# Kernel optimization log

Measured on AMD Instinct MI355X. Metric: run time of the kernel, lower is better.

## Reference

```python
import jax, jax.numpy as jnp
import numpy as np


def _flip_sequences(inputs, lengths):
    # Keeps padding at the end while reversing the valid prefix (per example).
    T = inputs.shape[1]
    def one(x, L):
        return jnp.flip(jnp.roll(x, T - L, axis=0), axis=0)
    return jax.vmap(one)(inputs, lengths)


def _gru_direction(xy, mask, Wi, Wh, bi, bhn):
    # xy: [B,T,D], mask: [B,T] (True = padding -> carry old state)
    B = xy.shape[0]
    H = bhn.shape[0]
    h0 = jnp.zeros((B, H), xy.dtype)
    xs = jnp.moveaxis(xy, 1, 0)    # [T,B,D]
    ms = jnp.moveaxis(mask, 1, 0)  # [T,B]

    def step(h, inp):
        x_t, m_t = inp
        gi = x_t @ Wi + bi          # [B,3H] input projections (r,z,n)
        gh = h @ Wh                 # [B,3H] hidden projections
        gi_r, gi_z, gi_n = jnp.split(gi, 3, axis=-1)
        gh_r, gh_z, gh_n = jnp.split(gh, 3, axis=-1)
        r = jax.nn.sigmoid(gi_r + gh_r)
        z = jax.nn.sigmoid(gi_z + gh_z)
        n = jnp.tanh(gi_n + r * (gh_n + bhn))
        new_h = (1.0 - z) * n + z * h
        h_next = jnp.where(m_t[:, None], h, new_h)  # mask: keep old state on padding
        return h_next, new_h

    _, outs = jax.lax.scan(step, h0, (xs, ms))
    return jnp.moveaxis(outs, 0, 1)  # [B,T,H]


def setup_inputs() -> dict:
    key = jax.random.key(0)
    ks = jax.random.split(key, 12)
    B, T, N, E, H = 256, 1000, 128, 4, 256
    D = N + E
    s = 0.08
    return {
        "spike_inputs": jax.random.normal(ks[0], (B, T, N), jnp.float32),
        "external_inputs": jax.random.normal(ks[1], (B, T, E), jnp.float32),
        "trial_lengths": jax.random.randint(ks[2], (B,), 1, T + 1),
        "Wi_f": jax.random.normal(ks[3], (D, 3 * H), jnp.float32) * s,
        "Wh_f": jax.random.normal(ks[4], (H, 3 * H), jnp.float32) * s,
        "bi_f": jnp.zeros((3 * H,), jnp.float32),
        "bhn_f": jnp.zeros((H,), jnp.float32),
        "Wi_b": jax.random.normal(ks[5], (D, 3 * H), jnp.float32) * s,
        "Wh_b": jax.random.normal(ks[6], (H, 3 * H), jnp.float32) * s,
        "bi_b": jnp.zeros((3 * H,), jnp.float32),
        "bhn_b": jnp.zeros((H,), jnp.float32),
    }


def reference(spike_inputs, external_inputs, trial_lengths,
              Wi_f, Wh_f, bi_f, bhn_f, Wi_b, Wh_b, bi_b, bhn_b):
    B, T = spike_inputs.shape[:2]
    # mask_sequences: True where t >= trial length (padding)
    mask = jnp.arange(T)[None, :] >= trial_lengths[:, None]  # [B,T]

    # forward direction
    xy_f = jnp.concatenate([spike_inputs, external_inputs], axis=-1)
    fwd = _gru_direction(xy_f, mask, Wi_f, Wh_f, bi_f, bhn_f)

    # backward direction on flipped sequences (padding stays at the end,
    # so the padding mask is identical)
    rs = _flip_sequences(spike_inputs, trial_lengths)
    re = _flip_sequences(external_inputs, trial_lengths)
    xy_b = jnp.concatenate([rs, re], axis=-1)
    bwd = _gru_direction(xy_b, mask, Wi_b, Wh_b, bi_b, bhn_b)
    bwd = _flip_sequences(bwd, trial_lengths)

    return jnp.concatenate([fwd, bwd], axis=-1)  # [B,T,2H]
```

## Files before the change

### kernel.cpp

```cpp
#include <hip/hip_runtime.h>

#define T_SEQ 1000
#define NS 128
#define NE 4
#define DIN 132
#define G3 768
#define WGS 512

typedef __attribute__((ext_vector_type(8))) short short8;
typedef __attribute__((ext_vector_type(4))) float floatx4;

#define CNT_OFF 0
#define HX_OFF  131072
#define HX_BYTES (32*2*8192)
#define WS_ZERO_BYTES (HX_OFF + HX_BYTES)

#define MFMA16(a,b,c) __builtin_amdgcn_mfma_f32_16x16x32_bf16((a),(b),(c),0,0,0)

__device__ __forceinline__ unsigned short f2bf(float f){
  unsigned u = __float_as_uint(f);
  return (unsigned short)((u + 0x7FFFu + ((u>>16)&1u)) >> 16);
}
__device__ __forceinline__ float bf2f(unsigned short b){
  return __uint_as_float(((unsigned)b)<<16);
}
__device__ __forceinline__ unsigned long long ld64a(const void* p){
  return __hip_atomic_load((const unsigned long long*)p, __ATOMIC_RELAXED, __HIP_MEMORY_SCOPE_AGENT);
}
__device__ __forceinline__ void st32a(void* p, unsigned v){
  __hip_atomic_store((unsigned*)p, v, __ATOMIC_RELAXED, __HIP_MEMORY_SCOPE_AGENT);
}

__global__ __launch_bounds__(WGS, 1) void bigru3(
  const float* __restrict__ spike, const float* __restrict__ extin,
  const int* __restrict__ lens,
  const float* __restrict__ WiF, const float* __restrict__ WhF,
  const float* __restrict__ biF, const float* __restrict__ bhF,
  const float* __restrict__ WiB, const float* __restrict__ WhB,
  const float* __restrict__ biB, const float* __restrict__ bhB,
  float* __restrict__ out,
  unsigned* __restrict__ cnt, char* __restrict__ hx)
{
  const int tid = threadIdx.x;
  const int bid = blockIdx.x;
  const int g   = bid >> 2;
  const int s   = bid & 3;
  const int dir = g >> 4;
  const int b_base = (g & 15) << 4;
  const int w  = tid >> 6;
  const int l  = tid & 63;
  const int dg = w >> 1;
  const int ks = w & 1;
  const int col = l & 15;
  const int q   = l >> 4;
  const int jd  = s*64 + dg*16 + col;

  const float* Wi  = dir ? WiB : WiF;
  const float* Wh  = dir ? WhB : WhF;
  const float* bi  = dir ? biB : biF;
  const float* bhn = dir ? bhB : bhF;

  __shared__ __align__(16) char  ldsXb[2*5*64*16];
  __shared__ __align__(16) float ldsC[4][4][16][20];
  __shared__ int ldsL[16];

  unsigned* cg  = cnt + g*T_SEQ;
  char*     hxg = hx + (size_t)g*2*8192;

  if (tid < 16) ldsL[tid] = lens[b_base + tid];
  for (int i = tid; i < 2*320; i += WGS)
    *(floatx4*)(ldsXb + i*16) = floatx4{0.f,0.f,0.f,0.f};
  __syncthreads();

  const int q8 = q*8;
  short8 Bh[4][3][2];
  short8 Bx[3][3][2];
  #pragma unroll
  for (int hk=0; hk<4; ++hk){
    const int k0 = (ks*4+hk)*32 + q8;
    #pragma unroll
    for (int gt=0; gt<3; ++gt){
      const int c = gt*256 + jd;
      #pragma unroll
      for (int i=0;i<8;++i){
        float wv = Wh[(size_t)(k0+i)*G3 + c];
        unsigned short hb = f2bf(wv);
        Bh[hk][gt][0][i] = (short)hb;
        Bh[hk][gt][1][i] = (short)f2bf(wv - bf2f(hb));
      }
    }
  }
  #pragma unroll
  for (int xk=0; xk<3; ++xk){
    const bool xv = (ks==0) || (xk<2);
    const int kxg = (ks==0) ? xk : (3+xk);
    const int k0 = kxg*32 + q8;
    #pragma unroll
    for (int gt=0; gt<3; ++gt){
      const int c = gt*256 + jd;
      #pragma unroll
      for (int i=0;i<8;++i){
        float wv = (xv && (k0+i) < DIN) ? Wi[(size_t)(k0+i)*G3 + c] : 0.f;
        unsigned short hb = f2bf(wv);
        Bx[xk][gt][0][i] = (short)hb;
        Bx[xk][gt][1][i] = (short)f2bf(wv - bf2f(hb));
      }
    }
  }

  const float bir = bi[jd], biz = bi[256+jd], bin = bi[512+jd], bhv = bhn[jd];
  int   Lr[4];
  float hold[4];
  #pragma unroll
  for (int j=0;j<4;++j){ Lr[j] = ldsL[q*4+j]; hold[j] = 0.f; }

  auto xload = [&](int m, int tt)->float4{
    const int row = m/33, pk = m - row*33, k0 = pk*4;
    const int L = ldsL[row];
    int tp = dir ? (L-1-tt) : tt;
    if (tp < 0) tp += T_SEQ;
    const size_t xb = (size_t)(b_base+row)*T_SEQ + tp;
    if (k0 < NS) return *(const float4*)(spike + xb*NS + k0);
    return *(const float4*)(extin + xb*NE);
  };
  auto xstore = [&](int m, float4 v, int buf){
    const int row = m/33, pk = m - row*33, k0 = pk*4;
    const int kg = k0>>5, sub = (k0>>3)&3, ii = k0&7;
    const int off = buf*5120 + ((kg*64 + row + 16*sub)*8 + ii)*2;
    unsigned lo = (unsigned)f2bf(v.x) | (((unsigned)f2bf(v.y))<<16);
    unsigned hi = (unsigned)f2bf(v.z) | (((unsigned)f2bf(v.w))<<16);
    *(unsigned*)(ldsXb + off)     = lo;
    *(unsigned*)(ldsXb + off + 4) = hi;
  };

  {
    float4 a = xload(tid, 0);  xstore(tid, a, 0);
    if (tid < 16){ float4 b = xload(tid+512, 0); xstore(tid+512, b, 0); }
  }
  __syncthreads();

  const int r0 = dg*64 + l;

  for (int t=0; t<T_SEQ; ++t){
    const int cur = t & 1, nxt = cur ^ 1;

    float4 sx0, sx1, sx2;
    if (ks==0 && t < T_SEQ-1){
      sx0 = xload(r0, t+1);
      sx1 = xload(r0+256, t+1);
      if (r0 < 16) sx2 = xload(r0+512, t+1);
    }

    floatx4 aR={0.f,0.f,0.f,0.f}, aZ={0.f,0.f,0.f,0.f}, aNH={0.f,0.f,0.f,0.f}, aNX={0.f,0.f,0.f,0.f};
    if (ks==0){
      #pragma unroll
      for (int xk=0; xk<3; ++xk){
        const short8 a = *(const short8*)(ldsXb + (cur*320 + xk*64 + l)*16);
        aR  = MFMA16(a, Bx[xk][0][0], aR ); aZ  = MFMA16(a, Bx[xk][1][0], aZ ); aNX = MFMA16(a, Bx[xk][2][0], aNX);
        aR  = MFMA16(a, Bx[xk][0][1], aR ); aZ  = MFMA16(a, Bx[xk][1][1], aZ ); aNX = MFMA16(a, Bx[xk][2][1], aNX);
      }
    } else {
      #pragma unroll
      for (int xk=0; xk<2; ++xk){
        const short8 a = *(const short8*)(ldsXb + (cur*320 + (3+xk)*64 + l)*16);
        aR  = MFMA16(a, Bx[xk][0][0], aR ); aZ  = MFMA16(a, Bx[xk][1][0], aZ ); aNX = MFMA16(a, Bx[xk][2][0], aNX);
        aR  = MFMA16(a, Bx[xk][0][1], aR ); aZ  = MFMA16(a, Bx[xk][1][1], aZ ); aNX = MFMA16(a, Bx[xk][2][1], aNX);
      }
    }

    if (t > 0){
      const unsigned* cp = &cg[t-1];
      while (__hip_atomic_load(cp, __ATOMIC_RELAXED, __HIP_MEMORY_SCOPE_AGENT) < 16u)
        __builtin_amdgcn_s_sleep(1);
      asm volatile("" ::: "memory");
    }

    short8 hf[4];
    {
      const char* hsrc = hxg + nxt*8192;
      #pragma unroll
      for (int hk=0; hk<4; ++hk){
        const char* p = hsrc + (((ks*4+hk)*64 + l)*16);
        union { unsigned long long qq[2]; short8 v; } u;
        u.qq[0] = ld64a(p); u.qq[1] = ld64a(p+8);
        hf[hk] = u.v;
      }
    }

    #pragma unroll
    for (int hk=0; hk<4; ++hk){
      aR  = MFMA16(hf[hk], Bh[hk][0][0], aR ); aZ  = MFMA16(hf[hk], Bh[hk][1][0], aZ ); aNH = MFMA16(hf[hk], Bh[hk][2][0], aNH);
      aR  = MFMA16(hf[hk], Bh[hk][0][1], aR ); aZ  = MFMA16(hf[hk], Bh[hk][1][1], aZ ); aNH = MFMA16(hf[hk], Bh[hk][2][1], aNH);
    }

    if (ks==0){
      *(floatx4*)&ldsC[dg][0][col][q*4] = aR;
      *(floatx4*)&ldsC[dg][1][col][q*4] = aZ;
      *(floatx4*)&ldsC[dg][2][col][q*4] = aNH;
      *(floatx4*)&ldsC[dg][3][col][q*4] = aNX;
    }
    __syncthreads();

    if (ks==1){
      aR  += *(const floatx4*)&ldsC[dg][0][col][q*4];
      aZ  += *(const floatx4*)&ldsC[dg][1][col][q*4];
      aNH += *(const floatx4*)&ldsC[dg][2][col][q*4];
      aNX += *(const floatx4*)&ldsC[dg][3][col][q*4];
      unsigned dwj[4];
      #pragma unroll
      for (int j=0;j<4;++j){
        const int rj = q*4 + j;
        const float gr = aR[j] + bir;
        const float gz = aZ[j] + biz;
        const float r = __fdividef(1.f, 1.f + __expf(-gr));
        const float z = __fdividef(1.f, 1.f + __expf(-gz));
        float pn = aNX[j] + bin + r*(aNH[j] + bhv);
        pn = fminf(fmaxf(pn, -20.f), 20.f);
        const float e2 = __expf(-2.f*pn);
        const float n  = __fdividef(1.f - e2, 1.f + e2);
        const float hn  = (1.f - z)*n + z*hold[j];
        const float hnx = (t < Lr[j]) ? hn : hold[j];
        hold[j] = hnx;
        int tp = dir ? (Lr[j]-1-t) : t;
        if (tp < 0) tp += T_SEQ;
        out[((size_t)(b_base+rj)*T_SEQ + tp)*512 + dir*256 + jd] = hn;
        unsigned bf = f2bf(hnx);
        unsigned ot = (unsigned)__shfl_xor((int)bf, 1);
        dwj[j] = (l & 1) ? 0u : (bf | (ot << 16));
      }
      if (t < T_SEQ-1){
        if ((l & 1) == 0){
          const int kg = jd >> 5, d5 = jd & 31;
          char* dst = hxg + cur*8192 + ((kg*64 + 16*(d5>>3))*16 + (d5&7)*2);
          #pragma unroll
          for (int j=0;j<4;++j)
            st32a(dst + (q*4+j)*16, dwj[j]);
        }
        asm volatile("s_waitcnt vmcnt(0)" ::: "memory");
        if (l == 0)
          __hip_atomic_fetch_add(&cg[t], 1u, __ATOMIC_RELAXED, __HIP_MEMORY_SCOPE_AGENT);
      }
    } else {
      if (t < T_SEQ-1){
        xstore(r0, sx0, nxt);
        xstore(r0+256, sx1, nxt);
        if (r0 < 16) xstore(r0+512, sx2, nxt);
      }
    }
    __syncthreads();
  }
}

extern "C" void kernel_launch(void* const* d_in, const int* in_sizes, int n_in,
                              void* d_out, int out_size, void* d_ws, size_t ws_size,
                              hipStream_t stream) {
  (void)in_sizes; (void)n_in; (void)out_size; (void)ws_size;
  const float* spike = (const float*)d_in[0];
  const float* extin = (const float*)d_in[1];
  const int*   lens  = (const int*)  d_in[2];
  const float* WiF   = (const float*)d_in[3];
  const float* WhF   = (const float*)d_in[4];
  const float* biF   = (const float*)d_in[5];
  const float* bhF   = (const float*)d_in[6];
  const float* WiB   = (const float*)d_in[7];
  const float* WhB   = (const float*)d_in[8];
  const float* biB   = (const float*)d_in[9];
  const float* bhB   = (const float*)d_in[10];
  float* out = (float*)d_out;
  char* ws = (char*)d_ws;
  unsigned* cnt = (unsigned*)(ws + CNT_OFF);
  char*     hx  = ws + HX_OFF;

  hipMemsetAsync(ws, 0, WS_ZERO_BYTES, stream);
  bigru3<<<dim3(128), dim3(WGS), 0, stream>>>(
      spike, extin, lens, WiF, WhF, biF, bhF, WiB, WhB, biB, bhB, out, cnt, hx);
}
```

Before: 4.689 ms.

## Replace per-step atomic counters with per-wave timestamp flags and reorder stores

Each cross-workgroup step barrier used to be a per-timestep counter bumped with atomic fetch-add. Now each of the 16 producing waves writes its own monotonically increasing timestamp slot, and consumers poll all 16 slots with a wave ballot. This removes atomic read-modify-write contention and shrinks the workspace that needs zeroing. The output stores are moved after the flag publish so they no longer delay the signal, the next-step input prefetch is moved after the hidden-state load, and the launch bounds change to waves_per_eu(2,2), which could affect register allocation.

```diff
diff --git a/kernel.cpp b/kernel.cpp
--- a/kernel.cpp
+++ b/kernel.cpp
@@ -6,13 +6,14 @@
 #define DIN 132
 #define G3 768
 #define WGS 512
+#define NWG 128
 
 typedef __attribute__((ext_vector_type(8))) short short8;
 typedef __attribute__((ext_vector_type(4))) float floatx4;
 
-#define CNT_OFF 0
-#define HX_OFF  131072
-#define HX_BYTES (32*2*8192)
+#define STAMP_OFF 0
+#define HX_OFF    4096
+#define HX_BYTES  (32*2*8192)
 #define WS_ZERO_BYTES (HX_OFF + HX_BYTES)
 
 #define MFMA16(a,b,c) __builtin_amdgcn_mfma_f32_16x16x32_bf16((a),(b),(c),0,0,0)
@@ -27,19 +28,23 @@
 __device__ __forceinline__ unsigned long long ld64a(const void* p){
   return __hip_atomic_load((const unsigned long long*)p, __ATOMIC_RELAXED, __HIP_MEMORY_SCOPE_AGENT);
 }
+__device__ __forceinline__ unsigned ld32a(const void* p){
+  return __hip_atomic_load((const unsigned*)p, __ATOMIC_RELAXED, __HIP_MEMORY_SCOPE_AGENT);
+}
 __device__ __forceinline__ void st32a(void* p, unsigned v){
   __hip_atomic_store((unsigned*)p, v, __ATOMIC_RELAXED, __HIP_MEMORY_SCOPE_AGENT);
 }
 
-__global__ __launch_bounds__(WGS, 1) void bigru3(
+__global__ __launch_bounds__(WGS)
+__attribute__((amdgpu_waves_per_eu(2, 2)))
+void bigru6(
   const float* __restrict__ spike, const float* __restrict__ extin,
   const int* __restrict__ lens,
   const float* __restrict__ WiF, const float* __restrict__ WhF,
   const float* __restrict__ biF, const float* __restrict__ bhF,
   const float* __restrict__ WiB, const float* __restrict__ WhB,
   const float* __restrict__ biB, const float* __restrict__ bhB,
-  float* __restrict__ out,
-  unsigned* __restrict__ cnt, char* __restrict__ hx)
+  float* __restrict__ out, char* __restrict__ ws)
 {
   const int tid = threadIdx.x;
   const int bid = blockIdx.x;
@@ -64,8 +69,8 @@
   __shared__ __align__(16) float ldsC[4][4][16][20];
   __shared__ int ldsL[16];
 
-  unsigned* cg  = cnt + g*T_SEQ;
-  char*     hxg = hx + (size_t)g*2*8192;
+  unsigned* stg = (unsigned*)(ws + STAMP_OFF) + g*16;
+  char*     hxg = ws + HX_OFF + (size_t)g*2*8192;
 
   if (tid < 16) ldsL[tid] = lens[b_base + tid];
   for (int i = tid; i < 2*320; i += WGS)
@@ -140,51 +145,56 @@
   __syncthreads();
 
   const int r0 = dg*64 + l;
+  const int kg_o = jd >> 5, d5 = jd & 31;
+  const int wslot = s*4 + dg;
 
   for (int t=0; t<T_SEQ; ++t){
     const int cur = t & 1, nxt = cur ^ 1;
+
+    floatx4 aR={0.f,0.f,0.f,0.f}, aZ={0.f,0.f,0.f,0.f}, aNH={0.f,0.f,0.f,0.f}, aNX={0.f,0.f,0.f,0.f};
+    if (ks==0){
+      #pragma unroll
+      for (int xk=0; xk<3; ++xk){
+        const short8 a = *(const short8*)(ldsXb + (cur*320 + xk*64 + l)*16);
+        aR  = MFMA16(a, Bx[xk][0][0], aR ); aZ  = MFMA16(a, Bx[xk][1][0], aZ ); aNX = MFMA16(a, Bx[xk][2][0], aNX);
+        aR  = MFMA16(a, Bx[xk][0][1], aR ); aZ  = MFMA16(a, Bx[xk][1][1], aZ ); aNX = MFMA16(a, Bx[xk][2][1], aNX);
+      }
+    } else {
+      #pragma unroll
+      for (int xk=0; xk<2; ++xk){
+        const short8 a = *(const short8*)(ldsXb + (cur*320 + (3+xk)*64 + l)*16);
+        aR  = MFMA16(a, Bx[xk][0][0], aR ); aZ  = MFMA16(a, Bx[xk][1][0], aZ ); aNX = MFMA16(a, Bx[xk][2][0], aNX);
+        aR  = MFMA16(a, Bx[xk][0][1], aR ); aZ  = MFMA16(a, Bx[xk][1][1], aZ ); aNX = MFMA16(a, Bx[xk][2][1], aNX);
+      }
+    }
+
+    if (t > 0){
+      const unsigned* sp = stg + (l & 15);
+      while (true){
+        unsigned v = ld32a(sp);
+        if (__ballot(v >= (unsigned)t) == ~0ull) break;
+        __builtin_amdgcn_s_sleep(1);
+      }
+      asm volatile("" ::: "memory");
+    }
+
+    short8 hf[4];
+    {
+      const char* hsrc = hxg + nxt*8192;
+      #pragma unroll
+      for (int hk=0; hk<4; ++hk){
+        const char* p = hsrc + (((ks*4+hk)*64 + l)*16);
+        union { unsigned long long qq[2]; short8 v; } u;
+        u.qq[0] = ld64a(p); u.qq[1] = ld64a(p+8);
+        hf[hk] = u.v;
+      }
+    }
 
     float4 sx0, sx1, sx2;
     if (ks==0 && t < T_SEQ-1){
       sx0 = xload(r0, t+1);
       sx1 = xload(r0+256, t+1);
       if (r0 < 16) sx2 = xload(r0+512, t+1);
-    }
-
-    floatx4 aR={0.f,0.f,0.f,0.f}, aZ={0.f,0.f,0.f,0.f}, aNH={0.f,0.f,0.f,0.f}, aNX={0.f,0.f,0.f,0.f};
-    if (ks==0){
-      #pragma unroll
-      for (int xk=0; xk<3; ++xk){
-        const short8 a = *(const short8*)(ldsXb + (cur*320 + xk*64 + l)*16);
-        aR  = MFMA16(a, Bx[xk][0][0], aR ); aZ  = MFMA16(a, Bx[xk][1][0], aZ ); aNX = MFMA16(a, Bx[xk][2][0], aNX);
-        aR  = MFMA16(a, Bx[xk][0][1], aR ); aZ  = MFMA16(a, Bx[xk][1][1], aZ ); aNX = MFMA16(a, Bx[xk][2][1], aNX);
-      }
-    } else {
-      #pragma unroll
-      for (int xk=0; xk<2; ++xk){
-        const short8 a = *(const short8*)(ldsXb + (cur*320 + (3+xk)*64 + l)*16);
-        aR  = MFMA16(a, Bx[xk][0][0], aR ); aZ  = MFMA16(a, Bx[xk][1][0], aZ ); aNX = MFMA16(a, Bx[xk][2][0], aNX);
-        aR  = MFMA16(a, Bx[xk][0][1], aR ); aZ  = MFMA16(a, Bx[xk][1][1], aZ ); aNX = MFMA16(a, Bx[xk][2][1], aNX);
-      }
-    }
-
-    if (t > 0){
-      const unsigned* cp = &cg[t-1];
-      while (__hip_atomic_load(cp, __ATOMIC_RELAXED, __HIP_MEMORY_SCOPE_AGENT) < 16u)
-        __builtin_amdgcn_s_sleep(1);
-      asm volatile("" ::: "memory");
-    }
-
-    short8 hf[4];
-    {
-      const char* hsrc = hxg + nxt*8192;
-      #pragma unroll
-      for (int hk=0; hk<4; ++hk){
-        const char* p = hsrc + (((ks*4+hk)*64 + l)*16);
-        union { unsigned long long qq[2]; short8 v; } u;
-        u.qq[0] = ld64a(p); u.qq[1] = ld64a(p+8);
-        hf[hk] = u.v;
-      }
     }
 
     #pragma unroll
@@ -207,9 +217,9 @@
       aNH += *(const floatx4*)&ldsC[dg][2][col][q*4];
       aNX += *(const floatx4*)&ldsC[dg][3][col][q*4];
       unsigned dwj[4];
+      float hnv[4];
       #pragma unroll
       for (int j=0;j<4;++j){
-        const int rj = q*4 + j;
         const float gr = aR[j] + bir;
         const float gz = aZ[j] + biz;
         const float r = __fdividef(1.f, 1.f + __expf(-gr));
@@ -221,24 +231,29 @@
         const float hn  = (1.f - z)*n + z*hold[j];
         const float hnx = (t < Lr[j]) ? hn : hold[j];
         hold[j] = hnx;
-        int tp = dir ? (Lr[j]-1-t) : t;
-        if (tp < 0) tp += T_SEQ;
-        out[((size_t)(b_base+rj)*T_SEQ + tp)*512 + dir*256 + jd] = hn;
+        hnv[j] = hn;
         unsigned bf = f2bf(hnx);
         unsigned ot = (unsigned)__shfl_xor((int)bf, 1);
         dwj[j] = (l & 1) ? 0u : (bf | (ot << 16));
       }
       if (t < T_SEQ-1){
         if ((l & 1) == 0){
-          const int kg = jd >> 5, d5 = jd & 31;
-          char* dst = hxg + cur*8192 + ((kg*64 + 16*(d5>>3))*16 + (d5&7)*2);
+          char* dst = hxg + cur*8192 + ((kg_o*64 + 16*(d5>>3))*16 + (d5&7)*2);
           #pragma unroll
           for (int j=0;j<4;++j)
             st32a(dst + (q*4+j)*16, dwj[j]);
         }
         asm volatile("s_waitcnt vmcnt(0)" ::: "memory");
+        __builtin_amdgcn_sched_barrier(0);
         if (l == 0)
-          __hip_atomic_fetch_add(&cg[t], 1u, __ATOMIC_RELAXED, __HIP_MEMORY_SCOPE_AGENT);
+          st32a(stg + wslot, (unsigned)(t+1));
+      }
+      #pragma unroll
+      for (int j=0;j<4;++j){
+        const int rj = q*4 + j;
+        int tp = dir ? (Lr[j]-1-t) : t;
+        if (tp < 0) tp += T_SEQ;
+        out[((size_t)(b_base+rj)*T_SEQ + tp)*512 + dir*256 + jd] = hnv[j];
       }
     } else {
       if (t < T_SEQ-1){
@@ -268,10 +283,8 @@
   const float* bhB   = (const float*)d_in[10];
   float* out = (float*)d_out;
   char* ws = (char*)d_ws;
-  unsigned* cnt = (unsigned*)(ws + CNT_OFF);
-  char*     hx  = ws + HX_OFF;
 
   hipMemsetAsync(ws, 0, WS_ZERO_BYTES, stream);
-  bigru3<<<dim3(128), dim3(WGS), 0, stream>>>(
-      spike, extin, lens, WiF, WhF, biF, bhF, WiB, WhB, biB, bhB, out, cnt, hx);
-}
+  bigru6<<<dim3(NWG), dim3(WGS), 0, stream>>>(
+      spike, extin, lens, WiF, WhF, biF, bhF, WiB, WhB, biB, bhB, out, ws);
+}
```

Result: slower. 4.811 ms (+2.6%).
